# Performance work log

Hardware: AMD Instinct MI355X
Metric: run time of the kernel (lower is better)

The kernel has to match this reference:

```python
import math
import jax, jax.numpy as jnp
import numpy as np

DIM = 1024
HID = 2048  # int(dim * expansion_factor)
QK = 128
G = 256     # group size
B, N = 4, 4096
NUM_BUCKETS = 32
MAX_DIST = 128


def _rel_pos_bias(rel_emb, g, scale):
    # non-causal T5 relative position bucket (num_buckets halved to 16)
    pos = jnp.arange(g)
    rel = pos[None, :] - pos[:, None]          # k_pos - q_pos
    n = -rel
    nb = NUM_BUCKETS // 2                       # 16
    ret = (n < 0).astype(jnp.int32) * nb
    n = jnp.abs(n)
    max_exact = nb // 2                         # 8
    is_small = n < max_exact
    val_large = max_exact + (
        jnp.log(jnp.maximum(n, 1).astype(jnp.float32) / max_exact)
        / math.log(MAX_DIST / max_exact) * (nb - max_exact)
    ).astype(jnp.int32)
    val_large = jnp.minimum(val_large, nb - 1)
    bucket = ret + jnp.where(is_small, n, val_large)   # [g, g] in [0, 32)
    return rel_emb[bucket, 0] * scale                   # [g, g]


def _layernorm(x, g, b, eps=1e-5):
    mu = jnp.mean(x, axis=-1, keepdims=True)
    var = jnp.mean((x - mu) ** 2, axis=-1, keepdims=True)
    return (x - mu) * jax.lax.rsqrt(var + eps) * g + b


def setup_inputs() -> dict:
    key = jax.random.key(0)
    ks = jax.random.split(key, 8)
    return {
        "x": jax.random.normal(ks[0], (B, N, DIM), dtype=jnp.float32),
        "ln_g": jnp.ones((DIM,), jnp.float32),
        "ln_b": jnp.zeros((DIM,), jnp.float32),
        "W_h": jax.random.normal(ks[1], (DIM, 2 * HID), jnp.float32) * 0.02,
        "b_h": jnp.zeros((2 * HID,), jnp.float32),
        "W_qk": jax.random.normal(ks[2], (DIM, QK), jnp.float32) * 0.02,
        "b_qk": jnp.zeros((QK,), jnp.float32),
        "os_gamma": jax.random.normal(ks[3], (4, QK), jnp.float32) * 0.02,
        "os_beta": jnp.zeros((4, QK), jnp.float32),
        "rel_emb": jax.random.normal(ks[4], (NUM_BUCKETS, 1), jnp.float32) * 0.02,
        "W_out": jax.random.normal(ks[5], (HID, DIM), jnp.float32) * 0.02,
        "b_out": jnp.zeros((DIM,), jnp.float32),
    }


def reference(x, ln_g, ln_b, W_h, b_h, W_qk, b_qk, os_gamma, os_beta, rel_emb, W_out, b_out):
    b, n = x.shape[0], x.shape[1]
    ng = n // G
    normed = _layernorm(x, ln_g, ln_b)
    hid = jax.nn.silu(normed @ W_h + b_h)               # [b, n, 2*HID]
    v, gate = hid[..., :HID], hid[..., HID:]
    qk = jax.nn.silu(normed @ W_qk + b_qk)              # [b, n, QK]
    # OffsetScale heads=4 -> quad_q, lin_q, quad_k, lin_k
    heads = qk[..., None, :] * os_gamma + os_beta        # [b, n, 4, QK]
    quad_q, lin_q, quad_k, lin_k = [heads[..., h, :] for h in range(4)]
    # group into blocks of G
    def grp(t):
        return t.reshape(b, ng, G, t.shape[-1])
    quad_q, quad_k, lin_q, lin_k, vg = map(grp, (quad_q, quad_k, lin_q, lin_k, v))
    # quadratic (local) branch: ReLU^2 attention per group + T5 bias
    sim = jnp.einsum('bgid,bgjd->bgij', quad_q, quad_k) / G
    sim = sim + _rel_pos_bias(rel_emb, G, QK ** 0.5)
    attn = jax.nn.relu(sim) ** 2
    quad_out = jnp.einsum('bgij,bgje->bgie', attn, vg)   # [b, ng, G, HID]
    # linear (global) branch, reduced over groups (non-causal)
    lin_kv = jnp.einsum('bgnd,bgne->bde', lin_k, vg) / n
    lin_out = jnp.einsum('bde,bgnd->bgne', lin_kv, lin_q)
    out = (quad_out + lin_out).reshape(b, n, HID)
    out = gate * out
    return out @ W_out + b_out + x
```

## Files before the change

### kernel.cpp

```cpp
#include <hip/hip_runtime.h>
#include <hip/hip_bf16.h>


typedef __attribute__((ext_vector_type(8))) short short8;
typedef __attribute__((ext_vector_type(4))) float f32x4;

#define BM 128
#define BN 128
#define BK 32

struct Aux {
  const float* b1;
  const float* x;
  const float* gamma;
  const float* beta;
  const float* biastab;
  const unsigned short* a2;
  const unsigned short* bkv;
  const unsigned short* gate;
  unsigned short* o16a;
  unsigned short* o16b;
  unsigned short* o16c;
  unsigned short* o16d;
  float* o32;
};

__device__ __forceinline__ float bf2f(unsigned short u) {
  union { float f; unsigned int i; } w; w.i = ((unsigned int)u) << 16; return w.f;
}
__device__ __forceinline__ unsigned short f2bf(float f) {
  union { float f; unsigned int i; } w; w.f = f;
  unsigned int x = w.i;
  return (unsigned short)((x + 0x7FFFu + ((x >> 16) & 1u)) >> 16);
}
__device__ __forceinline__ float silu_f(float z) { return z / (1.0f + __expf(-z)); }

__device__ __forceinline__ void async_cp16(const unsigned short* g, unsigned short* l) {
  __builtin_amdgcn_global_load_lds(
      (const __attribute__((address_space(1))) void*)g,
      (__attribute__((address_space(3))) void*)l, 16, 0, 0);
}

__device__ __forceinline__ float block_sum(float v) {
  #pragma unroll
  for (int o = 32; o > 0; o >>= 1) v += __shfl_down(v, o, 64);
  __shared__ float sh[4];
  __syncthreads();
  if ((threadIdx.x & 63) == 0) sh[threadIdx.x >> 6] = v;
  __syncthreads();
  return sh[0] + sh[1] + sh[2] + sh[3];
}

__global__ __launch_bounds__(256) void ln_k(const float* __restrict__ x,
                                            const float* __restrict__ g,
                                            const float* __restrict__ b,
                                            unsigned short* __restrict__ out) {
  const int row = blockIdx.x;
  const int tid = threadIdx.x;
  const float4 xv = ((const float4*)(x + (size_t)row * 1024))[tid];
  float s = xv.x + xv.y + xv.z + xv.w;
  s = block_sum(s);
  const float mu = s * (1.0f / 1024.0f);
  const float d0 = xv.x - mu, d1 = xv.y - mu, d2 = xv.z - mu, d3 = xv.w - mu;
  float q = d0 * d0 + d1 * d1 + d2 * d2 + d3 * d3;
  q = block_sum(q);
  const float rstd = rsqrtf(q * (1.0f / 1024.0f) + 1e-5f);
  const float4 gv = ((const float4*)g)[tid];
  const float4 bv = ((const float4*)b)[tid];
  unsigned short* o = out + (size_t)row * 1024 + tid * 4;
  o[0] = f2bf(d0 * rstd * gv.x + bv.x);
  o[1] = f2bf(d1 * rstd * gv.y + bv.y);
  o[2] = f2bf(d2 * rstd * gv.z + bv.z);
  o[3] = f2bf(d3 * rstd * gv.w + bv.w);
}

__global__ __launch_bounds__(256) void tc_k(const float* __restrict__ in,
                                            unsigned short* __restrict__ out,
                                            int K, int N) {
  __shared__ unsigned short L[64][65];
  const int t = threadIdx.x;
  const int k0 = blockIdx.y * 64, n0 = blockIdx.x * 64;
  const int r = t >> 4, c4 = (t & 15) * 4;
  #pragma unroll
  for (int rr = 0; rr < 4; ++rr) {
    const int kk = rr * 16 + r;
    const float4 f = ((const float4*)(in + (size_t)(k0 + kk) * N + n0))[t & 15];
    L[kk][c4 + 0] = f2bf(f.x); L[kk][c4 + 1] = f2bf(f.y);
    L[kk][c4 + 2] = f2bf(f.z); L[kk][c4 + 3] = f2bf(f.w);
  }
  __syncthreads();
  #pragma unroll
  for (int rr = 0; rr < 4; ++rr) {
    const int nn = rr * 16 + r;
    ushort4 u;
    u.x = L[c4 + 0][nn]; u.y = L[c4 + 1][nn];
    u.z = L[c4 + 2][nn]; u.w = L[c4 + 3][nn];
    ((ushort4*)(out + (size_t)(n0 + nn) * K + k0))[t & 15] = u;
  }
}

__global__ void bias_k(const float* __restrict__ rel, float* __restrict__ tab) {
  int idx = blockIdx.x * 256 + threadIdx.x;
  if (idx >= 511) return;
  int d = idx - 255;
  int n = -d;
  int ret = (n < 0) ? 16 : 0;
  int a = (n < 0) ? -n : n;
  int bucket;
  if (a < 8) {
    bucket = ret + a;
  } else {
    float t = __logf((float)a * 0.125f) / 2.7725887298583984f * 8.0f;
    int vl = 8 + (int)t;
    if (vl > 15) vl = 15;
    bucket = ret + vl;
  }
  tab[idx] = rel[bucket] * 11.313708498984761f;
}

__global__ void kvred_k(const float* __restrict__ pkv, unsigned short* __restrict__ linkvT) {
  int i4 = blockIdx.x * 256 + threadIdx.x;
  const int b = i4 >> 16, rem = i4 & 65535;
  const float4* p = (const float4*)(pkv + (size_t)b * 1048576) + rem;
  const float4 p0 = p[0], p1 = p[65536], p2 = p[131072], p3 = p[196608];
  ushort4 u;
  u.x = f2bf((p0.x + p1.x + p2.x + p3.x) * (1.0f / 4096.0f));
  u.y = f2bf((p0.y + p1.y + p2.y + p3.y) * (1.0f / 4096.0f));
  u.z = f2bf((p0.z + p1.z + p2.z + p3.z) * (1.0f / 4096.0f));
  u.w = f2bf((p0.w + p1.w + p2.w + p3.w) * (1.0f / 4096.0f));
  ((ushort4*)(linkvT + (size_t)b * 262144))[rem] = u;
}

template<int MODE>
__global__ __launch_bounds__(256, 2) void gemm_k(
    const unsigned short* __restrict__ Ag,
    const unsigned short* __restrict__ Bg,
    int lda, int ldb, int kiters, Aux aux)
{
  __shared__ unsigned short As[BM * BK];
  __shared__ unsigned short Bs[BN * BK];

  const int tid  = threadIdx.x;
  const int lane = tid & 63;
  const int wave = tid >> 6;
  const int quad = lane >> 4;
  const int l16  = lane & 15;
  const int wm   = (wave >> 1) * 64;
  const int wn   = (wave & 1) * 64;
  const int bz   = blockIdx.z;
  const int bm   = blockIdx.y * BM;
  const int bn   = blockIdx.x * BN;

  const unsigned short* A = Ag;
  const unsigned short* B = Bg;
  if constexpr (MODE == 2) { A += (size_t)bz * 32768;  B += (size_t)bz * 32768; }
  if constexpr (MODE == 3) { A += (size_t)bz * 65536;
                             B += (size_t)(bz >> 4) * 8388608 + (size_t)(bz & 15) * 256; }
  if constexpr (MODE == 4) { const int b = bz >> 2, s = bz & 3;
                             A += (size_t)b * 524288 + (size_t)s * 1024;
                             B += (size_t)b * 8388608 + (size_t)s * 1024; }

  const unsigned short* A2 = nullptr;
  const unsigned short* B2 = nullptr;
  if constexpr (MODE == 3) {
    A2 = aux.a2 + (size_t)bz * 32768;
    B2 = aux.bkv + (size_t)(bz >> 4) * 262144;
  }

  const int srow = wave * 32 + (lane >> 2);
  const int scol = (lane & 3) * 8;
  unsigned short* lA = As + wave * 1024;
  unsigned short* lB = Bs + wave * 1024;

  const f32x4 zero = {0.f, 0.f, 0.f, 0.f};
  f32x4 acc[4][4];
  #pragma unroll
  for (int i = 0; i < 4; ++i)
    #pragma unroll
    for (int j = 0; j < 4; ++j) acc[i][j] = zero;

  for (int kt = 0; kt < kiters; ++kt) {
    const unsigned short* pa = A;
    const unsigned short* pb = B;
    int la = lda, lb = ldb, kk = kt * BK;
    if constexpr (MODE == 3) {
      if (kt >= 8) { pa = A2; pb = B2; la = 128; lb = 128; kk -= 256; }
    }

    __syncthreads();
    async_cp16(pa + (size_t)(bm + srow) * la + kk + scol, lA);
    async_cp16(pa + (size_t)(bm + srow + 16) * la + kk + scol, lA + 512);
    async_cp16(pb + (size_t)(bn + srow) * lb + kk + scol, lB);
    async_cp16(pb + (size_t)(bn + srow + 16) * lb + kk + scol, lB + 512);
    __syncthreads();

    short8 af[4], bfv[4];
    #pragma unroll
    for (int i = 0; i < 4; ++i)
      af[i] = *reinterpret_cast<const short8*>(As + (wm + i * 16 + l16) * BK + quad * 8);
    #pragma unroll
    for (int j = 0; j < 4; ++j)
      bfv[j] = *reinterpret_cast<const short8*>(Bs + (wn + j * 16 + l16) * BK + quad * 8);

    #pragma unroll
    for (int i = 0; i < 4; ++i)
      #pragma unroll
      for (int j = 0; j < 4; ++j)
        acc[i][j] = __builtin_amdgcn_mfma_f32_16x16x32_bf16(af[i], bfv[j], acc[i][j], 0, 0, 0);
  }

  #pragma unroll
  for (int i = 0; i < 4; ++i) {
    #pragma unroll
    for (int j = 0; j < 4; ++j) {
      const int row0 = bm + wm + i * 16 + quad * 4;
      const int col  = bn + wn + j * 16 + l16;
      if constexpr (MODE == 0) {
        const float bb = aux.b1[col];
        float s[4];
        #pragma unroll
        for (int r = 0; r < 4; ++r) s[r] = silu_f(acc[i][j][r] + bb);
        if (col < 2048) {
          const int b = row0 >> 12, t = row0 & 4095;
          ushort4 u; u.x = f2bf(s[0]); u.y = f2bf(s[1]); u.z = f2bf(s[2]); u.w = f2bf(s[3]);
          *(ushort4*)(aux.o16a + (size_t)b * 8388608 + (size_t)col * 4096 + t) = u;
        } else {
          #pragma unroll
          for (int r = 0; r < 4; ++r)
            aux.o16b[(size_t)(row0 + r) * 2048 + (col - 2048)] = f2bf(s[r]);
        }
      } else if constexpr (MODE == 1) {
        const float bb = aux.b1[col];
        float s[4];
        #pragma unroll
        for (int r = 0; r < 4; ++r) s[r] = silu_f(acc[i][j][r] + bb);
        #pragma unroll
        for (int r = 0; r < 4; ++r) {
          const size_t idx = (size_t)(row0 + r) * 128 + col;
          aux.o16a[idx] = f2bf(s[r] * aux.gamma[col]       + aux.beta[col]);
          aux.o16b[idx] = f2bf(s[r] * aux.gamma[128 + col] + aux.beta[128 + col]);
          aux.o16c[idx] = f2bf(s[r] * aux.gamma[256 + col] + aux.beta[256 + col]);
        }
        const int b = row0 >> 12, t = row0 & 4095;
        const float g4 = aux.gamma[384 + col], b4 = aux.beta[384 + col];
        ushort4 u;
        u.x = f2bf(s[0] * g4 + b4); u.y = f2bf(s[1] * g4 + b4);
        u.z = f2bf(s[2] * g4 + b4); u.w = f2bf(s[3] * g4 + b4);
        *(ushort4*)(aux.o16d + (size_t)b * 524288 + (size_t)col * 4096 + t) = u;
      } else if constexpr (MODE == 2) {
        #pragma unroll
        for (int r = 0; r < 4; ++r) {
          float s = acc[i][j][r] * (1.0f / 256.0f) + aux.biastab[col - (row0 + r) + 255];
          s = fmaxf(s, 0.0f);
          aux.o16a[(size_t)bz * 65536 + (size_t)(row0 + r) * 256 + col] = f2bf(s * s);
        }
      } else if constexpr (MODE == 3) {
        #pragma unroll
        for (int r = 0; r < 4; ++r) {
          const size_t idx = ((size_t)bz * 256 + row0 + r) * 2048 + col;
          aux.o16a[idx] = f2bf(acc[i][j][r] * bf2f(aux.gate[idx]));
        }
      } else if constexpr (MODE == 4) {
        float4 u; u.x = acc[i][j][0]; u.y = acc[i][j][1]; u.z = acc[i][j][2]; u.w = acc[i][j][3];
        *(float4*)(aux.o32 + (size_t)bz * 262144 + (size_t)col * 128 + row0) = u;
      } else if constexpr (MODE == 6) {
        #pragma unroll
        for (int r = 0; r < 4; ++r) {
          const size_t idx = (size_t)(row0 + r) * 1024 + col;
          aux.o32[idx] = acc[i][j][r] + aux.b1[col] + aux.x[idx];
        }
      }
    }
  }
}

extern "C" void kernel_launch(void* const* d_in, const int* in_sizes, int n_in,
                              void* d_out, int out_size, void* d_ws, size_t ws_size,
                              hipStream_t stream) {
  (void)in_sizes; (void)n_in; (void)out_size; (void)ws_size;
  const float* x     = (const float*)d_in[0];
  const float* ln_g  = (const float*)d_in[1];
  const float* ln_b  = (const float*)d_in[2];
  const float* W_h   = (const float*)d_in[3];
  const float* b_h   = (const float*)d_in[4];
  const float* W_qk  = (const float*)d_in[5];
  const float* b_qk  = (const float*)d_in[6];
  const float* osg   = (const float*)d_in[7];
  const float* osb   = (const float*)d_in[8];
  const float* rel   = (const float*)d_in[9];
  const float* W_out = (const float*)d_in[10];
  const float* b_out = (const float*)d_in[11];
  float* out = (float*)d_out;

  char* w = (char*)d_ws;
  size_t off = 0;
  auto alloc = [&](size_t bytes) { char* p = w + off; off += (bytes + 255) & ~(size_t)255; return p; };

  unsigned short* normed = (unsigned short*)alloc(16384ull * 1024 * 2);
  unsigned short* whT    = (unsigned short*)alloc(4096ull * 1024 * 2);
  unsigned short* qq     = (unsigned short*)alloc(16384ull * 128 * 2);
  unsigned short* qkk    = (unsigned short*)alloc(16384ull * 128 * 2);
  unsigned short* linkT  = (unsigned short*)alloc(4ull * 128 * 4096 * 2);
  float*          pkvT   = (float*)alloc(16ull * 2048 * 128 * 4);
  unsigned short* wqkT   = (unsigned short*)alloc(128ull * 1024 * 2);
  unsigned short* woutT  = (unsigned short*)alloc(1024ull * 2048 * 2);
  unsigned short* vT     = (unsigned short*)alloc(4ull * 2048 * 4096 * 2);
  unsigned short* gate   = (unsigned short*)alloc(16384ull * 2048 * 2);
  unsigned short* lq     = (unsigned short*)alloc(16384ull * 128 * 2);
  unsigned short* attn   = (unsigned short*)alloc(64ull * 256 * 256 * 2);
  unsigned short* linkvT = (unsigned short*)alloc(4ull * 2048 * 128 * 2);
  float*          btab   = (float*)alloc(511 * 4);
  unsigned short* gated  = (unsigned short*)w;

  tc_k<<<dim3(64, 16), 256, 0, stream>>>(W_h,   whT,   1024, 4096);
  tc_k<<<dim3(2, 16),  256, 0, stream>>>(W_qk,  wqkT,  1024, 128);
  tc_k<<<dim3(16, 32), 256, 0, stream>>>(W_out, woutT, 2048, 1024);
  bias_k<<<2, 256, 0, stream>>>(rel, btab);
  ln_k<<<16384, 256, 0, stream>>>(x, ln_g, ln_b, normed);

  Aux a0{}; a0.b1 = b_h; a0.o16a = vT; a0.o16b = gate;
  gemm_k<0><<<dim3(32, 128, 1), 256, 0, stream>>>(normed, whT, 1024, 1024, 32, a0);

  Aux a1{}; a1.b1 = b_qk; a1.gamma = osg; a1.beta = osb;
  a1.o16a = qq; a1.o16b = lq; a1.o16c = qkk; a1.o16d = linkT;
  gemm_k<1><<<dim3(1, 128, 1), 256, 0, stream>>>(normed, wqkT, 1024, 1024, 32, a1);

  Aux a2x{}; a2x.biastab = btab; a2x.o16a = attn;
  gemm_k<2><<<dim3(2, 2, 64), 256, 0, stream>>>(qq, qkk, 128, 128, 4, a2x);

  Aux a4{}; a4.o32 = pkvT;
  gemm_k<4><<<dim3(16, 1, 16), 256, 0, stream>>>(linkT, vT, 4096, 4096, 8, a4);

  kvred_k<<<1024, 256, 0, stream>>>(pkvT, linkvT);

  Aux a3{}; a3.a2 = lq; a3.bkv = linkvT; a3.gate = gate; a3.o16a = gated;
  gemm_k<3><<<dim3(16, 2, 64), 256, 0, stream>>>(attn, vT, 256, 4096, 12, a3);

  Aux a6{}; a6.b1 = b_out; a6.x = x; a6.o32 = out;
  gemm_k<6><<<dim3(8, 128, 1), 256, 0, stream>>>(gated, woutT, 2048, 2048, 64, a6);
}
```

Baseline: 596.3 us.

## Double GEMM K-tile to 64 and fuse QK projection into hidden GEMM

The GEMM K-tile grows from 32 to 64, so each block makes half as many barrier-synchronised load/compute iterations, and the loop now issues two MFMA sub-steps per tile. The W_qk projection is folded into the W_h GEMM by concatenating the transposed weights into one 4224-column matrix. The epilogue branches by column to produce either v/gate or the four offset-scaled QK heads. This removes a separate 128-block launch and a second read of the normalized activations, at the cost of double LDS use per block, which may lower occupancy.

```diff
diff --git a/kernel.cpp b/kernel.cpp
--- a/kernel.cpp
+++ b/kernel.cpp
@@ -7,10 +7,11 @@
 
 #define BM 128
 #define BN 128
-#define BK 32
+#define BK 64
 
 struct Aux {
   const float* b1;
+  const float* b2;
   const float* x;
   const float* gamma;
   const float* beta;
@@ -22,6 +23,8 @@
   unsigned short* o16b;
   unsigned short* o16c;
   unsigned short* o16d;
+  unsigned short* o16e;
+  unsigned short* o16f;
   float* o32;
 };
 
@@ -167,10 +170,10 @@
     B2 = aux.bkv + (size_t)(bz >> 4) * 262144;
   }
 
-  const int srow = wave * 32 + (lane >> 2);
-  const int scol = (lane & 3) * 8;
-  unsigned short* lA = As + wave * 1024;
-  unsigned short* lB = Bs + wave * 1024;
+  const int srow = wave * 8 + (lane >> 3);
+  const int scol = (lane & 7) * 8;
+  unsigned short* lA = As + wave * 512;
+  unsigned short* lB = Bs + wave * 512;
 
   const f32x4 zero = {0.f, 0.f, 0.f, 0.f};
   f32x4 acc[4][4];
@@ -184,29 +187,32 @@
     const unsigned short* pb = B;
     int la = lda, lb = ldb, kk = kt * BK;
     if constexpr (MODE == 3) {
-      if (kt >= 8) { pa = A2; pb = B2; la = 128; lb = 128; kk -= 256; }
+      if (kt >= 4) { pa = A2; pb = B2; la = 128; lb = 128; kk -= 256; }
     }
 
     __syncthreads();
-    async_cp16(pa + (size_t)(bm + srow) * la + kk + scol, lA);
-    async_cp16(pa + (size_t)(bm + srow + 16) * la + kk + scol, lA + 512);
-    async_cp16(pb + (size_t)(bn + srow) * lb + kk + scol, lB);
-    async_cp16(pb + (size_t)(bn + srow + 16) * lb + kk + scol, lB + 512);
+    #pragma unroll
+    for (int i = 0; i < 4; ++i) {
+      async_cp16(pa + (size_t)(bm + i * 32 + srow) * la + kk + scol, lA + i * 2048);
+      async_cp16(pb + (size_t)(bn + i * 32 + srow) * lb + kk + scol, lB + i * 2048);
+    }
     __syncthreads();
 
-    short8 af[4], bfv[4];
     #pragma unroll
-    for (int i = 0; i < 4; ++i)
-      af[i] = *reinterpret_cast<const short8*>(As + (wm + i * 16 + l16) * BK + quad * 8);
-    #pragma unroll
-    for (int j = 0; j < 4; ++j)
-      bfv[j] = *reinterpret_cast<const short8*>(Bs + (wn + j * 16 + l16) * BK + quad * 8);
-
-    #pragma unroll
-    for (int i = 0; i < 4; ++i)
+    for (int kh = 0; kh < 2; ++kh) {
+      short8 af[4], bfv[4];
+      #pragma unroll
+      for (int i = 0; i < 4; ++i)
+        af[i] = *reinterpret_cast<const short8*>(As + (wm + i * 16 + l16) * BK + kh * 32 + quad * 8);
       #pragma unroll
       for (int j = 0; j < 4; ++j)
-        acc[i][j] = __builtin_amdgcn_mfma_f32_16x16x32_bf16(af[i], bfv[j], acc[i][j], 0, 0, 0);
+        bfv[j] = *reinterpret_cast<const short8*>(Bs + (wn + j * 16 + l16) * BK + kh * 32 + quad * 8);
+      #pragma unroll
+      for (int i = 0; i < 4; ++i)
+        #pragma unroll
+        for (int j = 0; j < 4; ++j)
+          acc[i][j] = __builtin_amdgcn_mfma_f32_16x16x32_bf16(af[i], bfv[j], acc[i][j], 0, 0, 0);
+    }
   }
 
   #pragma unroll
@@ -216,37 +222,40 @@
       const int row0 = bm + wm + i * 16 + quad * 4;
       const int col  = bn + wn + j * 16 + l16;
       if constexpr (MODE == 0) {
-        const float bb = aux.b1[col];
-        float s[4];
-        #pragma unroll
-        for (int r = 0; r < 4; ++r) s[r] = silu_f(acc[i][j][r] + bb);
-        if (col < 2048) {
+        if (col < 4096) {
+          const float bb = aux.b1[col];
+          float s[4];
+          #pragma unroll
+          for (int r = 0; r < 4; ++r) s[r] = silu_f(acc[i][j][r] + bb);
+          if (col < 2048) {
+            const int b = row0 >> 12, t = row0 & 4095;
+            ushort4 u; u.x = f2bf(s[0]); u.y = f2bf(s[1]); u.z = f2bf(s[2]); u.w = f2bf(s[3]);
+            *(ushort4*)(aux.o16a + (size_t)b * 8388608 + (size_t)col * 4096 + t) = u;
+          } else {
+            #pragma unroll
+            for (int r = 0; r < 4; ++r)
+              aux.o16b[(size_t)(row0 + r) * 2048 + (col - 2048)] = f2bf(s[r]);
+          }
+        } else {
+          const int cq = col - 4096;
+          const float bb = aux.b2[cq];
+          float s[4];
+          #pragma unroll
+          for (int r = 0; r < 4; ++r) s[r] = silu_f(acc[i][j][r] + bb);
+          #pragma unroll
+          for (int r = 0; r < 4; ++r) {
+            const size_t idx = (size_t)(row0 + r) * 128 + cq;
+            aux.o16c[idx] = f2bf(s[r] * aux.gamma[cq]       + aux.beta[cq]);
+            aux.o16d[idx] = f2bf(s[r] * aux.gamma[128 + cq] + aux.beta[128 + cq]);
+            aux.o16e[idx] = f2bf(s[r] * aux.gamma[256 + cq] + aux.beta[256 + cq]);
+          }
           const int b = row0 >> 12, t = row0 & 4095;
-          ushort4 u; u.x = f2bf(s[0]); u.y = f2bf(s[1]); u.z = f2bf(s[2]); u.w = f2bf(s[3]);
-          *(ushort4*)(aux.o16a + (size_t)b * 8388608 + (size_t)col * 4096 + t) = u;
-        } else {
-          #pragma unroll
-          for (int r = 0; r < 4; ++r)
-            aux.o16b[(size_t)(row0 + r) * 2048 + (col - 2048)] = f2bf(s[r]);
+          const float g4 = aux.gamma[384 + cq], b4 = aux.beta[384 + cq];
+          ushort4 u;
+          u.x = f2bf(s[0] * g4 + b4); u.y = f2bf(s[1] * g4 + b4);
+          u.z = f2bf(s[2] * g4 + b4); u.w = f2bf(s[3] * g4 + b4);
+          *(ushort4*)(aux.o16f + (size_t)b * 524288 + (size_t)cq * 4096 + t) = u;
         }
-      } else if constexpr (MODE == 1) {
-        const float bb = aux.b1[col];
-        float s[4];
-        #pragma unroll
-        for (int r = 0; r < 4; ++r) s[r] = silu_f(acc[i][j][r] + bb);
-        #pragma unroll
-        for (int r = 0; r < 4; ++r) {
-          const size_t idx = (size_t)(row0 + r) * 128 + col;
-          aux.o16a[idx] = f2bf(s[r] * aux.gamma[col]       + aux.beta[col]);
-          aux.o16b[idx] = f2bf(s[r] * aux.gamma[128 + col] + aux.beta[128 + col]);
-          aux.o16c[idx] = f2bf(s[r] * aux.gamma[256 + col] + aux.beta[256 + col]);
-        }
-        const int b = row0 >> 12, t = row0 & 4095;
-        const float g4 = aux.gamma[384 + col], b4 = aux.beta[384 + col];
-        ushort4 u;
-        u.x = f2bf(s[0] * g4 + b4); u.y = f2bf(s[1] * g4 + b4);
-        u.z = f2bf(s[2] * g4 + b4); u.w = f2bf(s[3] * g4 + b4);
-        *(ushort4*)(aux.o16d + (size_t)b * 524288 + (size_t)col * 4096 + t) = u;
       } else if constexpr (MODE == 2) {
         #pragma unroll
         for (int r = 0; r < 4; ++r) {
@@ -297,12 +306,11 @@
   auto alloc = [&](size_t bytes) { char* p = w + off; off += (bytes + 255) & ~(size_t)255; return p; };
 
   unsigned short* normed = (unsigned short*)alloc(16384ull * 1024 * 2);
-  unsigned short* whT    = (unsigned short*)alloc(4096ull * 1024 * 2);
+  unsigned short* whqkT  = (unsigned short*)alloc(4224ull * 1024 * 2);
   unsigned short* qq     = (unsigned short*)alloc(16384ull * 128 * 2);
   unsigned short* qkk    = (unsigned short*)alloc(16384ull * 128 * 2);
   unsigned short* linkT  = (unsigned short*)alloc(4ull * 128 * 4096 * 2);
   float*          pkvT   = (float*)alloc(16ull * 2048 * 128 * 4);
-  unsigned short* wqkT   = (unsigned short*)alloc(128ull * 1024 * 2);
   unsigned short* woutT  = (unsigned short*)alloc(1024ull * 2048 * 2);
   unsigned short* vT     = (unsigned short*)alloc(4ull * 2048 * 4096 * 2);
   unsigned short* gate   = (unsigned short*)alloc(16384ull * 2048 * 2);
@@ -312,30 +320,27 @@
   float*          btab   = (float*)alloc(511 * 4);
   unsigned short* gated  = (unsigned short*)w;
 
-  tc_k<<<dim3(64, 16), 256, 0, stream>>>(W_h,   whT,   1024, 4096);
-  tc_k<<<dim3(2, 16),  256, 0, stream>>>(W_qk,  wqkT,  1024, 128);
+  tc_k<<<dim3(64, 16), 256, 0, stream>>>(W_h,   whqkT,              1024, 4096);
+  tc_k<<<dim3(2, 16),  256, 0, stream>>>(W_qk,  whqkT + 4096 * 1024, 1024, 128);
   tc_k<<<dim3(16, 32), 256, 0, stream>>>(W_out, woutT, 2048, 1024);
   bias_k<<<2, 256, 0, stream>>>(rel, btab);
   ln_k<<<16384, 256, 0, stream>>>(x, ln_g, ln_b, normed);
 
-  Aux a0{}; a0.b1 = b_h; a0.o16a = vT; a0.o16b = gate;
-  gemm_k<0><<<dim3(32, 128, 1), 256, 0, stream>>>(normed, whT, 1024, 1024, 32, a0);
-
-  Aux a1{}; a1.b1 = b_qk; a1.gamma = osg; a1.beta = osb;
-  a1.o16a = qq; a1.o16b = lq; a1.o16c = qkk; a1.o16d = linkT;
-  gemm_k<1><<<dim3(1, 128, 1), 256, 0, stream>>>(normed, wqkT, 1024, 1024, 32, a1);
+  Aux a0{}; a0.b1 = b_h; a0.b2 = b_qk; a0.gamma = osg; a0.beta = osb;
+  a0.o16a = vT; a0.o16b = gate; a0.o16c = qq; a0.o16d = lq; a0.o16e = qkk; a0.o16f = linkT;
+  gemm_k<0><<<dim3(33, 128, 1), 256, 0, stream>>>(normed, whqkT, 1024, 1024, 16, a0);
 
   Aux a2x{}; a2x.biastab = btab; a2x.o16a = attn;
-  gemm_k<2><<<dim3(2, 2, 64), 256, 0, stream>>>(qq, qkk, 128, 128, 4, a2x);
+  gemm_k<2><<<dim3(2, 2, 64), 256, 0, stream>>>(qq, qkk, 128, 128, 2, a2x);
 
   Aux a4{}; a4.o32 = pkvT;
-  gemm_k<4><<<dim3(16, 1, 16), 256, 0, stream>>>(linkT, vT, 4096, 4096, 8, a4);
+  gemm_k<4><<<dim3(16, 1, 16), 256, 0, stream>>>(linkT, vT, 4096, 4096, 4, a4);
 
   kvred_k<<<1024, 256, 0, stream>>>(pkvT, linkvT);
 
   Aux a3{}; a3.a2 = lq; a3.bkv = linkvT; a3.gate = gate; a3.o16a = gated;
-  gemm_k<3><<<dim3(16, 2, 64), 256, 0, stream>>>(attn, vT, 256, 4096, 12, a3);
+  gemm_k<3><<<dim3(16, 2, 64), 256, 0, stream>>>(attn, vT, 256, 4096, 6, a3);
 
   Aux a6{}; a6.b1 = b_out; a6.x = x; a6.o32 = out;
-  gemm_k<6><<<dim3(8, 128, 1), 256, 0, stream>>>(gated, woutT, 2048, 2048, 64, a6);
-}
+  gemm_k<6><<<dim3(8, 128, 1), 256, 0, stream>>>(gated, woutT, 2048, 2048, 32, a6);
+}
```

New measurement: 630.5 us. 1.06x slower.
